# Performance work log

Hardware: AMD Instinct MI355X
Metric: run time of the kernel (lower is better)

The kernel has to match this reference:

```python
import jax, jax.numpy as jnp
import numpy as np
import math

L = 6; D = 768; NH = 12; DH = D // NH; V = 2048; CTX = 512; B = 16; T = 512
PAD_ID = 0; PAD_X = 18; PAD_Y = 32; N_ACTIONS = 9


def _layernorm(x, s, b, eps=1e-5):
    m = jnp.mean(x, axis=-1, keepdims=True)
    v = jnp.mean((x - m) ** 2, axis=-1, keepdims=True)
    return (x - m) * jax.lax.rsqrt(v + eps) * s + b


def setup_inputs() -> dict:
    key = jax.random.key(0)
    ks = jax.random.split(key, 16)
    s = 0.02
    x_emb = jax.random.normal(ks[4], (19, D), jnp.float32) * s
    x_emb = x_emb.at[PAD_X].set(0.0)  # padding_idx row is zero in torch
    y_emb = jax.random.normal(ks[5], (33, D), jnp.float32) * s
    y_emb = y_emb.at[PAD_Y].set(0.0)
    return {
        "history_cards": jax.random.randint(ks[0], (B, T), 0, V),
        "history_players": jax.random.randint(ks[1], (B, T), 0, 2),
        "deck": jax.random.randint(ks[2], (B, 8), 0, V),
        "opp_deck": jax.random.randint(ks[3], (B, 8), 0, V),
        "tok_emb": jax.random.normal(ks[6], (V, D), jnp.float32) * s,
        "player_emb": jax.random.normal(ks[7], (2, D), jnp.float32) * s,
        "pos_emb": jax.random.normal(ks[8], (CTX, D), jnp.float32) * s,
        "x_emb": x_emb,
        "y_emb": y_emb,
        "ln1_s": jnp.ones((L, D), jnp.float32),
        "ln1_b": jnp.zeros((L, D), jnp.float32),
        "qkv_w": jax.random.normal(ks[9], (L, D, 3 * D), jnp.float32) * s,
        "qkv_b": jnp.zeros((L, 3 * D), jnp.float32),
        "proj_w": jax.random.normal(ks[10], (L, D, D), jnp.float32) * s,
        "proj_b": jnp.zeros((L, D), jnp.float32),
        "ln2_s": jnp.ones((L, D), jnp.float32),
        "ln2_b": jnp.zeros((L, D), jnp.float32),
        "fc1_w": jax.random.normal(ks[11], (L, D, 4 * D), jnp.float32) * s,
        "fc1_b": jnp.zeros((L, 4 * D), jnp.float32),
        "fc2_w": jax.random.normal(ks[12], (L, 4 * D, D), jnp.float32) * s,
        "fc2_b": jnp.zeros((L, D), jnp.float32),
        "lnf_s": jnp.ones((D,), jnp.float32),
        "lnf_b": jnp.zeros((D,), jnp.float32),
        "head_w": jax.random.normal(ks[13], (D, N_ACTIONS), jnp.float32) * s,
        "head_b": jnp.zeros((N_ACTIONS,), jnp.float32),
    }


def reference(history_cards, history_players, deck, opp_deck,
              tok_emb, player_emb, pos_emb, x_emb, y_emb,
              ln1_s, ln1_b, qkv_w, qkv_b, proj_w, proj_b,
              ln2_s, ln2_b, fc1_w, fc1_b, fc2_w, fc2_b,
              lnf_s, lnf_b, head_w, head_b):
    Bc, Tc = history_cards.shape
    attn_mask = history_cards != PAD_ID                      # (B,T) True = valid
    all_pad = ~jnp.any(attn_mask, axis=1)
    attn_mask = attn_mask.at[:, 0].set(attn_mask[:, 0] | all_pad)

    # multi-embedding sum (history_x/history_y are None => padding rows = 0)
    h = (tok_emb[history_cards]
         + player_emb[jnp.clip(history_players, 0, 1)]
         + x_emb[PAD_X] + y_emb[PAD_Y]
         + jnp.mean(tok_emb[deck], axis=1, keepdims=True)
         + jnp.mean(tok_emb[opp_deck], axis=1, keepdims=True))
    x = h + pos_emb[:Tc][None]                               # (B,T,D)

    causal = jnp.tril(jnp.ones((Tc, Tc), bool))
    mask = causal[None, None, :, :] & attn_mask[:, None, None, :]  # (B,1,T,T)
    neg_inf = jnp.float32(-jnp.inf)
    scale = 1.0 / math.sqrt(DH)

    for i in range(L):
        # attention
        xn = _layernorm(x, ln1_s[i], ln1_b[i])
        qkv = xn @ qkv_w[i] + qkv_b[i]
        q, k, v = jnp.split(qkv, 3, axis=-1)
        q = q.reshape(Bc, Tc, NH, DH)
        k = k.reshape(Bc, Tc, NH, DH)
        v = v.reshape(Bc, Tc, NH, DH)
        scores = jnp.einsum('bihd,bjhd->bhij', q, k) * scale
        scores = jnp.where(mask, scores, neg_inf)
        w = jax.nn.softmax(scores, axis=-1)
        w = jnp.nan_to_num(w, nan=0.0, posinf=0.0, neginf=0.0)
        y = jnp.einsum('bhij,bjhd->bihd', w, v).reshape(Bc, Tc, D)
        x = x + (y @ proj_w[i] + proj_b[i])
        # MLP
        xn = _layernorm(x, ln2_s[i], ln2_b[i])
        hmid = jax.nn.gelu(xn @ fc1_w[i] + fc1_b[i], approximate=False)
        x = x + (hmid @ fc2_w[i] + fc2_b[i])

    x = _layernorm(x, lnf_s, lnf_b)
    last_idx = jnp.clip(jnp.sum(attn_mask.astype(jnp.int32), axis=1) - 1, 0, None)
    last_h = x[jnp.arange(Bc), last_idx]                     # (B,D)
    return last_h @ head_w + head_b                          # (B,9)
```

## Files before the change

### kernel.cpp

```cpp
#include <hip/hip_runtime.h>
#include <hip/hip_bf16.h>
#include <math.h>

typedef __hip_bfloat16 bf16;
typedef __bf16 bf16x8 __attribute__((ext_vector_type(8)));
typedef float f32x4 __attribute__((ext_vector_type(4)));

__device__ __forceinline__ float b2f(bf16 v){ return __bfloat162float(v); }
__device__ __forceinline__ bf16  f2b(float v){ return __float2bfloat16(v); }

__device__ __forceinline__ float gelu_f(float v){
    float y = v * (1.f + 0.044715f * v * v);
    return v / (1.f + __expf(-1.5957691216057308f * y));
}

__device__ __forceinline__ void gl_lds16(const bf16* g, bf16* l) {
    __builtin_amdgcn_global_load_lds((const __attribute__((address_space(1))) unsigned int*)g,
                                     (__attribute__((address_space(3))) unsigned int*)l, 16, 0, 0);
}

__device__ __forceinline__ uint2 pack4bf(const float* v){
    union { unsigned short e[4]; uint2 u; } pk;
    #pragma unroll
    for (int r = 0; r < 4; r++) pk.e[r] = __builtin_bit_cast(unsigned short, f2b(v[r]));
    return pk.u;
}

__device__ __forceinline__ void phase_bar() {
    __builtin_amdgcn_sched_barrier(0);
    __builtin_amdgcn_s_barrier();
    __builtin_amdgcn_sched_barrier(0);
}

__global__ __launch_bounds__(256) void deckmean_k(const int* __restrict__ deck, const int* __restrict__ opp,
                                                  const float* __restrict__ tok, float* __restrict__ deckm)
{
    int b = blockIdx.x, w = blockIdx.y;
    const int* dk = (w ? opp : deck) + b * 8;
    int idx[8];
    #pragma unroll
    for (int j = 0; j < 8; j++) idx[j] = dk[j];
    float* out = deckm + (size_t)(w * 16 + b) * 768;
    for (int d = threadIdx.x; d < 768; d += 256) {
        float s = 0.f;
        #pragma unroll
        for (int j = 0; j < 8; j++) s += tok[(size_t)idx[j] * 768 + d];
        out[d] = s * 0.125f;
    }
}

__global__ __launch_bounds__(512) void mask_k(const int* __restrict__ cards, int* __restrict__ maskb,
                                              int* __restrict__ lastidx)
{
    int b = blockIdx.x, t = threadIdx.x;
    int m = (cards[b * 512 + t] != 0) ? 1 : 0;
    maskb[b * 512 + t] = m;
    __shared__ int red[512];
    red[t] = m; __syncthreads();
    for (int st = 256; st > 0; st >>= 1) { if (t < st) red[t] += red[t + st]; __syncthreads(); }
    if (t == 0) {
        int cnt = red[0];
        if (cnt == 0) { maskb[b * 512] = 1; cnt = 1; }
        lastidx[b] = cnt - 1;
    }
}

__global__ __launch_bounds__(256) void embed_k(const int* __restrict__ cards, const int* __restrict__ players,
                                               const float* __restrict__ tok, const float* __restrict__ pemb,
                                               const float* __restrict__ pos, const float* __restrict__ deckm,
                                               float* __restrict__ x)
{
    int t = blockIdx.x;
    int b = t >> 9, ti = t & 511;
    int cd = cards[t];
    int p = players[t]; p = p < 0 ? 0 : (p > 1 ? 1 : p);
    const float* tr  = tok  + (size_t)cd * 768;
    const float* pr  = pemb + (size_t)p  * 768;
    const float* po  = pos  + (size_t)ti * 768;
    const float* dm = deckm + (size_t)b * 768;
    const float* om = deckm + (size_t)(16 + b) * 768;
    float* xr = x + (size_t)t * 768;
    for (int d = threadIdx.x; d < 768; d += 256)
        xr[d] = tr[d] + pr[d] + po[d] + dm[d] + om[d];
}

__global__ __launch_bounds__(192) void ln_k(const float* __restrict__ x, const float* __restrict__ s,
                                            const float* __restrict__ b, bf16* __restrict__ out)
{
    int row = blockIdx.x, tid = threadIdx.x;
    float4 v = ((const float4*)(x + (size_t)row * 768))[tid];
    float sum = v.x + v.y + v.z + v.w;
    float sq  = v.x * v.x + v.y * v.y + v.z * v.z + v.w * v.w;
    #pragma unroll
    for (int off = 32; off > 0; off >>= 1) {
        sum += __shfl_xor(sum, off, 64);
        sq  += __shfl_xor(sq,  off, 64);
    }
    __shared__ float red[6];
    int wv = tid >> 6;
    if ((tid & 63) == 0) { red[wv] = sum; red[3 + wv] = sq; }
    __syncthreads();
    float S = red[0] + red[1] + red[2];
    float Q = red[3] + red[4] + red[5];
    float mean = S * (1.f / 768.f);
    float var  = Q * (1.f / 768.f) - mean * mean;
    float rstd = rsqrtf(var + 1e-5f);
    float4 sv = ((const float4*)s)[tid];
    float4 bv = ((const float4*)b)[tid];
    float o[4] = { (v.x - mean) * rstd * sv.x + bv.x, (v.y - mean) * rstd * sv.y + bv.y,
                   (v.z - mean) * rstd * sv.z + bv.z, (v.w - mean) * rstd * sv.w + bv.w };
    ((uint2*)(out + (size_t)row * 768))[tid] = pack4bf(o);
}

__global__ __launch_bounds__(256) void transpose4_k(const float* __restrict__ qw, const float* __restrict__ pw,
                                                    const float* __restrict__ f1, const float* __restrict__ f2,
                                                    bf16* __restrict__ oq, bf16* __restrict__ op,
                                                    bf16* __restrict__ o1, bf16* __restrict__ o2)
{
    int t = blockIdx.x;
    const float* in; bf16* out; int K, N, nbx;
    if (t < 432)       { in = qw; out = oq; K = 768;  N = 2304; nbx = 36; }
    else if (t < 576)  { in = pw; out = op; K = 768;  N = 768;  t -= 432;  nbx = 12; }
    else if (t < 1152) { in = f1; out = o1; K = 768;  N = 3072; t -= 576;  nbx = 48; }
    else               { in = f2; out = o2; K = 3072; N = 768;  t -= 1152; nbx = 12; }
    int n0 = (t % nbx) * 64, k0 = (t / nbx) * 64;
    int kq = threadIdx.x & 15, nq = threadIdx.x >> 4;
    float4 rr[4];
    #pragma unroll
    for (int r = 0; r < 4; r++)
        rr[r] = *(const float4*)&in[(size_t)(k0 + kq * 4 + r) * N + n0 + nq * 4];
    const float* fp = (const float*)rr;
    #pragma unroll
    for (int c = 0; c < 4; c++) {
        float v[4] = { fp[c], fp[4 + c], fp[8 + c], fp[12 + c] };
        *(uint2*)&out[(size_t)(n0 + nq * 4 + c) * K + k0 + kq * 4] = pack4bf(v);
    }
}

__global__ __launch_bounds__(512, 2) void gemm256_k(const bf16* __restrict__ A, const bf16* __restrict__ BT,
                                                    const float* __restrict__ bias, bf16* __restrict__ out,
                                                    int N, int K, int act, int nbn)
{
    __shared__ __align__(16) bf16 As0[256 * 64];
    __shared__ __align__(16) bf16 As1[256 * 64];
    __shared__ __align__(16) bf16 Bs0[256 * 64];
    __shared__ __align__(16) bf16 Bs1[256 * 64];

    const int tid  = threadIdx.x;
    const int lane = tid & 63, wid = tid >> 6;
    const int quad = lane >> 4, l16 = lane & 15;
    const int wr = wid >> 2, wc = wid & 3;
    const int cg0 = quad ^ (l16 & 7);
    const int cg1 = cg0 ^ 4;

    const int nwg  = gridDim.x;
    const int wgid = ((int)blockIdx.x & 7) * (nwg >> 3) + ((int)blockIdx.x >> 3);
    const int mt = wgid / nbn, nt = wgid - mt * nbn;
    const int m0 = mt * 256, n0 = nt * 256;

    const int srow = wid * 8 + (lane >> 3);
    const int scg  = (lane & 7) ^ (lane >> 3);
    const bf16* sa[4]; const bf16* sb[4];
    #pragma unroll
    for (int s = 0; s < 4; s++) {
        sa[s] = A  + (size_t)(m0 + s * 64 + srow) * K + scg * 8;
        sb[s] = BT + (size_t)(n0 + s * 64 + srow) * K + scg * 8;
    }

#define STG_A2(s, DST) gl_lds16(sa[s], &DST[((s) * 64 + wid * 8) * 64])
#define STG_B2(s, DST) gl_lds16(sb[s], &DST[((s) * 64 + wid * 8) * 64])
#define ADV { _Pragma("unroll") for (int s = 0; s < 4; s++) { sa[s] += 64; sb[s] += 64; } }
#define LD_B2(BV, cg, BC) { _Pragma("unroll") for (int ni = 0; ni < 4; ni++) \
    BV[ni] = __builtin_bit_cast(bf16x8, *(const uint4*)&BC[(wc * 64 + ni * 16 + l16) * 64 + (cg) * 8]); }
#define LD_A2(rb, cg, AC) { _Pragma("unroll") for (int mi = 0; mi < 4; mi++) \
    afv[mi] = __builtin_bit_cast(bf16x8, *(const uint4*)&AC[(wr * 128 + (rb) + mi * 16 + l16) * 64 + (cg) * 8]); }
#define MFMA16(MB, BV) { _Pragma("unroll") for (int mi = 0; mi < 4; mi++) \
    _Pragma("unroll") for (int ni = 0; ni < 4; ni++) \
        acc[(MB) + mi][ni] = __builtin_amdgcn_mfma_f32_16x16x32_bf16(BV[ni], afv[mi], acc[(MB) + mi][ni], 0, 0, 0); }

#define TILE256(AC, BC, AN, BN, PF) { \
    LD_B2(bfv0, cg0, BC); LD_A2(0, cg0, AC); \
    if (PF) { STG_B2(0, BN); STG_B2(1, BN); STG_B2(2, BN); STG_B2(3, BN); } \
    phase_bar(); \
    __builtin_amdgcn_s_setprio(1); MFMA16(0, bfv0); __builtin_amdgcn_s_setprio(0); \
    phase_bar(); \
    LD_B2(bfv1, cg1, BC); LD_A2(0, cg1, AC); \
    if (PF) { STG_A2(0, AN); STG_A2(2, AN); } \
    phase_bar(); \
    __builtin_amdgcn_s_setprio(1); MFMA16(0, bfv1); __builtin_amdgcn_s_setprio(0); \
    phase_bar(); \
    LD_A2(64, cg0, AC); \
    if (PF) { STG_A2(1, AN); STG_A2(3, AN); ADV; } \
    phase_bar(); \
    __builtin_amdgcn_s_setprio(1); MFMA16(4, bfv0); __builtin_amdgcn_s_setprio(0); \
    phase_bar(); \
    LD_A2(64, cg1, AC); \
    phase_bar(); \
    __builtin_amdgcn_s_setprio(1); MFMA16(4, bfv1); __builtin_amdgcn_s_setprio(0); \
    if (PF) { asm volatile("s_waitcnt vmcnt(0)" ::: "memory"); } \
    phase_bar(); }

    f32x4 acc[8][4] = {};
    const int NKT = K >> 6;

    STG_B2(0, Bs0); STG_B2(1, Bs0); STG_B2(2, Bs0); STG_B2(3, Bs0);
    STG_A2(0, As0); STG_A2(1, As0); STG_A2(2, As0); STG_A2(3, As0);
    ADV;
    asm volatile("s_waitcnt vmcnt(0)" ::: "memory");
    phase_bar();

    bf16x8 bfv0[4], bfv1[4], afv[4];
    #pragma unroll 1
    for (int kt2 = 0; kt2 < NKT; kt2 += 2) {
        { const bool pf = true;
          TILE256(As0, Bs0, As1, Bs1, pf); }
        { const bool pf = (kt2 + 2 < NKT);
          TILE256(As1, Bs1, As0, Bs0, pf); }
    }

    float4 bv[4];
    #pragma unroll
    for (int ni = 0; ni < 4; ni++)
        bv[ni] = *(const float4*)&bias[n0 + wc * 64 + ni * 16 + quad * 4];

    #pragma unroll
    for (int mi = 0; mi < 8; mi++) {
        const int m = m0 + wr * 128 + mi * 16 + l16;
        #pragma unroll
        for (int ni = 0; ni < 4; ni++) {
            const int nb2 = n0 + wc * 64 + ni * 16 + quad * 4;
            float v[4] = { acc[mi][ni][0] + bv[ni].x, acc[mi][ni][1] + bv[ni].y,
                           acc[mi][ni][2] + bv[ni].z, acc[mi][ni][3] + bv[ni].w };
            if (act) {
                #pragma unroll
                for (int r = 0; r < 4; r++) v[r] = gelu_f(v[r]);
            }
            *(uint2*)&out[(size_t)m * N + nb2] = pack4bf(v);
        }
    }
#undef STG_A2
#undef STG_B2
#undef ADV
#undef LD_B2
#undef LD_A2
#undef MFMA16
#undef TILE256
}

__global__ __launch_bounds__(512, 2) void gemmn128_k(const bf16* __restrict__ A, const bf16* __restrict__ BT,
                                                     const float* __restrict__ bias, float* __restrict__ x,
                                                     int N, int K, int nbn)
{
    __shared__ __align__(16) bf16 NA0[256 * 64];
    __shared__ __align__(16) bf16 NA1[256 * 64];
    __shared__ __align__(16) bf16 NA2[256 * 64];
    __shared__ __align__(16) bf16 NB0[128 * 64];
    __shared__ __align__(16) bf16 NB1[128 * 64];
    __shared__ __align__(16) bf16 NB2[128 * 64];

    const int tid  = threadIdx.x;
    const int lane = tid & 63, wid = tid >> 6;
    const int quad = lane >> 4, l16 = lane & 15;
    const int wr = wid >> 1, wc = wid & 1;
    const int cg0 = quad ^ (l16 & 7);
    const int cg1 = cg0 ^ 4;

    const int nwg  = gridDim.x;
    const int wgid = ((int)blockIdx.x & 7) * (nwg >> 3) + ((int)blockIdx.x >> 3);
    const int mt = wgid / nbn, nt = wgid - mt * nbn;
    const int m0 = mt * 256, n0 = nt * 128;

    const int srow = wid * 8 + (lane >> 3);
    const int scg  = (lane & 7) ^ (lane >> 3);
    const bf16* sa[4]; const bf16* sb[2];
    #pragma unroll
    for (int s = 0; s < 4; s++) sa[s] = A  + (size_t)(m0 + s * 64 + srow) * K + scg * 8;
    #pragma unroll
    for (int s = 0; s < 2; s++) sb[s] = BT + (size_t)(n0 + s * 64 + srow) * K + scg * 8;

#define NSTG6(NA, NB) { \
    gl_lds16(sa[0], &NA[(0 * 64 + wid * 8) * 64]); gl_lds16(sa[1], &NA[(1 * 64 + wid * 8) * 64]); \
    gl_lds16(sa[2], &NA[(2 * 64 + wid * 8) * 64]); gl_lds16(sa[3], &NA[(3 * 64 + wid * 8) * 64]); \
    gl_lds16(sb[0], &NB[(0 * 64 + wid * 8) * 64]); gl_lds16(sb[1], &NB[(1 * 64 + wid * 8) * 64]); }
#define NADV { _Pragma("unroll") for (int s = 0; s < 4; s++) sa[s] += 64; sb[0] += 64; sb[1] += 64; }
#define NLD(cg, NA, NB) { _Pragma("unroll") for (int i = 0; i < 4; i++) { \
    bfv[i] = __builtin_bit_cast(bf16x8, *(const uint4*)&NB[(wc * 64 + i * 16 + l16) * 64 + (cg) * 8]); \
    afv[i] = __builtin_bit_cast(bf16x8, *(const uint4*)&NA[(wr * 64 + i * 16 + l16) * 64 + (cg) * 8]); } }
#define NMFMA { _Pragma("unroll") for (int mi = 0; mi < 4; mi++) \
    _Pragma("unroll") for (int ni = 0; ni < 4; ni++) \
        acc[mi][ni] = __builtin_amdgcn_mfma_f32_16x16x32_bf16(bfv[ni], afv[mi], acc[mi][ni], 0, 0, 0); }
#define NITER(NAc, NBc, NAs, NBs) { \
    const bool pf = (kt + 2 < NKT); \
    NLD(cg0, NAc, NBc); \
    if (pf) { NSTG6(NAs, NBs); NADV; } \
    phase_bar(); \
    __builtin_amdgcn_s_setprio(1); NMFMA; __builtin_amdgcn_s_setprio(0); \
    phase_bar(); \
    NLD(cg1, NAc, NBc); \
    phase_bar(); \
    __builtin_amdgcn_s_setprio(1); NMFMA; __builtin_amdgcn_s_setprio(0); \
    if (pf)               { asm volatile("s_waitcnt vmcnt(6)" ::: "memory"); phase_bar(); } \
    else if (kt + 1 < NKT){ asm volatile("s_waitcnt vmcnt(0)" ::: "memory"); phase_bar(); } \
    kt++; \
}

    f32x4 acc[4][4] = {};
    const int NKT = K >> 6;

    NSTG6(NA0, NB0); NADV;
    NSTG6(NA1, NB1); NADV;
    asm volatile("s_waitcnt vmcnt(6)" ::: "memory");
    phase_bar();

    int kt = 0;
    bf16x8 bfv[4], afv[4];
    #pragma unroll 1
    for (int kt3 = 0; kt3 < NKT; kt3 += 3) {
        NITER(NA0, NB0, NA2, NB2);
        NITER(NA1, NB1, NA0, NB0);
        NITER(NA2, NB2, NA1, NB1);
    }

    float4 bv4[4];
    #pragma unroll
    for (int ni = 0; ni < 4; ni++)
        bv4[ni] = *(const float4*)&bias[n0 + wc * 64 + ni * 16 + quad * 4];

    #pragma unroll
    for (int mi = 0; mi < 4; mi++) {
        const int m = m0 + wr * 64 + mi * 16 + l16;
        #pragma unroll
        for (int ni = 0; ni < 4; ni++) {
            const int nb2 = n0 + wc * 64 + ni * 16 + quad * 4;
            float* xp = &x[(size_t)m * N + nb2];
            float4 xo = *(float4*)xp;
            xo.x += acc[mi][ni][0] + bv4[ni].x;
            xo.y += acc[mi][ni][1] + bv4[ni].y;
            xo.z += acc[mi][ni][2] + bv4[ni].z;
            xo.w += acc[mi][ni][3] + bv4[ni].w;
            *(float4*)xp = xo;
        }
    }
#undef NSTG6
#undef NADV
#undef NLD
#undef NMFMA
#undef NITER
}

__global__ __launch_bounds__(256) void attn_k(const bf16* __restrict__ qkv, const int* __restrict__ mask,
                                              bf16* __restrict__ y)
{
    const int qt = blockIdx.x, h = blockIdx.y, b = blockIdx.z;
    const int qbase = qt * 128, tokb = b * 512;
    __shared__ __align__(16) unsigned short Kl[128][72];
    __shared__ __align__(16) unsigned short Vt[64][136];
    __shared__ __align__(16) unsigned short Ptq[4][16][136];
    __shared__ float mkf[128];

    const int tid = threadIdx.x, wave = tid >> 6, lane = tid & 63;
    const int quad = lane >> 4, l16 = lane & 15;

    bf16x8 bq[2][2];
    #pragma unroll
    for (int qc = 0; qc < 2; qc++) {
        const bf16* qp = &qkv[(size_t)(tokb + qbase + wave * 32 + qc * 16 + l16) * 2304 + h * 64];
        bq[qc][0] = __builtin_bit_cast(bf16x8, *(const uint4*)(qp + quad * 8));
        bq[qc][1] = __builtin_bit_cast(bf16x8, *(const uint4*)(qp + 32 + quad * 8));
    }

    float m_i[2] = { -INFINITY, -INFINITY }, l_i[2] = { 0.f, 0.f };
    f32x4 Oacc[2][4] = {};

    const int nst = qt + 1;
    for (int s = 0; s < nst; s++) {
        const int j0 = s * 128;
        __syncthreads();
        {
            int key = tid >> 1, c0 = (tid & 1) * 32;
            const bf16* kg = &qkv[(size_t)(tokb + j0 + key) * 2304 + 768  + h * 64 + c0];
            const bf16* vg = &qkv[(size_t)(tokb + j0 + key) * 2304 + 1536 + h * 64 + c0];
            #pragma unroll
            for (int q = 0; q < 4; q++)
                *(uint4*)&Kl[key][c0 + q * 8] = *(const uint4*)(kg + q * 8);
            union { uint4 u[4]; unsigned short e[32]; } vv;
            #pragma unroll
            for (int q = 0; q < 4; q++) vv.u[q] = *(const uint4*)(vg + q * 8);
            #pragma unroll
            for (int j = 0; j < 32; j++) Vt[c0 + j][key] = vv.e[j];
            if (tid < 128) mkf[tid] = mask[b * 512 + j0 + tid] ? 0.f : -INFINITY;
        }
        __syncthreads();

        #pragma unroll
        for (int qc = 0; qc < 2; qc++) {
            const int qi = qbase + wave * 32 + qc * 16 + l16;

            f32x4 sc[8] = {};
            #pragma unroll
            for (int kcc = 0; kcc < 8; kcc++) {
                bf16x8 af0 = __builtin_bit_cast(bf16x8, *(const uint4*)&Kl[kcc * 16 + l16][quad * 8]);
                bf16x8 af1 = __builtin_bit_cast(bf16x8, *(const uint4*)&Kl[kcc * 16 + l16][32 + quad * 8]);
                sc[kcc] = __builtin_amdgcn_mfma_f32_16x16x32_bf16(af0, bq[qc][0], sc[kcc], 0, 0, 0);
                sc[kcc] = __builtin_amdgcn_mfma_f32_16x16x32_bf16(af1, bq[qc][1], sc[kcc], 0, 0, 0);
            }

            float pv[8][4];
            float mx = -INFINITY;
            #pragma unroll
            for (int kcc = 0; kcc < 8; kcc++) {
                float4 mk4 = *(const float4*)&mkf[kcc * 16 + quad * 4];
                float mkr[4] = { mk4.x, mk4.y, mk4.z, mk4.w };
                #pragma unroll
                for (int r = 0; r < 4; r++) {
                    int krel = kcc * 16 + quad * 4 + r;
                    float sval = (j0 + krel <= qi) ? (sc[kcc][r] * 0.125f + mkr[r]) : -INFINITY;
                    pv[kcc][r] = sval;
                    mx = fmaxf(mx, sval);
                }
            }
            mx = fmaxf(mx, __shfl_xor(mx, 16, 64));
            mx = fmaxf(mx, __shfl_xor(mx, 32, 64));
            float mn = fmaxf(m_i[qc], mx);
            float alpha = (mn == -INFINITY) ? 1.f : __expf(m_i[qc] - mn);
            float lsum = 0.f;
            #pragma unroll
            for (int kcc = 0; kcc < 8; kcc++)
                #pragma unroll
                for (int r = 0; r < 4; r++) {
                    float pp = (pv[kcc][r] == -INFINITY) ? 0.f : __expf(pv[kcc][r] - mn);
                    pv[kcc][r] = pp; lsum += pp;
                }
            lsum += __shfl_xor(lsum, 16, 64);
            lsum += __shfl_xor(lsum, 32, 64);
            m_i[qc] = mn; l_i[qc] = alpha * l_i[qc] + lsum;

            #pragma unroll
            for (int kcc = 0; kcc < 8; kcc++)
                *(uint2*)&Ptq[wave][l16][kcc * 16 + quad * 4] = pack4bf(pv[kcc]);
            #pragma unroll
            for (int mc = 0; mc < 4; mc++)
                #pragma unroll
                for (int r = 0; r < 4; r++) Oacc[qc][mc][r] *= alpha;

            __syncthreads();

            #pragma unroll
            for (int kcc = 0; kcc < 4; kcc++) {
                bf16x8 pb = __builtin_bit_cast(bf16x8, *(const uint4*)&Ptq[wave][l16][kcc * 32 + quad * 8]);
                #pragma unroll
                for (int mc = 0; mc < 4; mc++) {
                    bf16x8 vf = __builtin_bit_cast(bf16x8, *(const uint4*)&Vt[mc * 16 + l16][kcc * 32 + quad * 8]);
                    Oacc[qc][mc] = __builtin_amdgcn_mfma_f32_16x16x32_bf16(vf, pb, Oacc[qc][mc], 0, 0, 0);
                }
            }
        }
    }

    #pragma unroll
    for (int qc = 0; qc < 2; qc++) {
        float inv = (l_i[qc] > 0.f) ? 1.f / l_i[qc] : 0.f;
        const int tok = tokb + qbase + wave * 32 + qc * 16 + l16;
        #pragma unroll
        for (int mc = 0; mc < 4; mc++) {
            float v[4] = { Oacc[qc][mc][0] * inv, Oacc[qc][mc][1] * inv,
                           Oacc[qc][mc][2] * inv, Oacc[qc][mc][3] * inv };
            *(uint2*)&y[(size_t)tok * 768 + h * 64 + mc * 16 + quad * 4] = pack4bf(v);
        }
    }
}

__global__ __launch_bounds__(256) void head_k(const float* __restrict__ x, const int* __restrict__ lastidx,
                                              const float* __restrict__ ls, const float* __restrict__ lb,
                                              const float* __restrict__ hw, const float* __restrict__ hb,
                                              float* __restrict__ out)
{
    int b = blockIdx.x, tid = threadIdx.x;
    const float* xr = x + ((size_t)(b * 512 + lastidx[b])) * 768;
    float v0 = xr[tid], v1 = xr[tid + 256], v2 = xr[tid + 512];
    __shared__ float rs[256], rq[256];
    rs[tid] = v0 + v1 + v2; rq[tid] = v0 * v0 + v1 * v1 + v2 * v2;
    __syncthreads();
    for (int st = 128; st > 0; st >>= 1) {
        if (tid < st) { rs[tid] += rs[tid + st]; rq[tid] += rq[tid + st]; }
        __syncthreads();
    }
    float mean = rs[0] * (1.f / 768.f);
    float var  = rq[0] * (1.f / 768.f) - mean * mean;
    float rstd = rsqrtf(var + 1e-5f);
    float part[9];
    #pragma unroll
    for (int a = 0; a < 9; a++) part[a] = 0.f;
    float vv[3] = { v0, v1, v2 };
    #pragma unroll
    for (int e = 0; e < 3; e++) {
        int d = tid + e * 256;
        float xnv = (vv[e] - mean) * rstd * ls[d] + lb[d];
        #pragma unroll
        for (int a = 0; a < 9; a++) part[a] += xnv * hw[d * 9 + a];
    }
    __shared__ float r9[9][256];
    #pragma unroll
    for (int a = 0; a < 9; a++) r9[a][tid] = part[a];
    __syncthreads();
    for (int st = 128; st > 0; st >>= 1) {
        if (tid < st) {
            for (int a = 0; a < 9; a++) r9[a][tid] += r9[a][tid + st];
        }
        __syncthreads();
    }
    if (tid < 9) out[b * 9 + tid] = r9[tid][0] + hb[tid];
}

extern "C" void kernel_launch(void* const* d_in, const int* in_sizes, int n_in,
                              void* d_out, int out_size, void* d_ws, size_t ws_size,
                              hipStream_t stream) {
    const int*   cards   = (const int*)  d_in[0];
    const int*   players = (const int*)  d_in[1];
    const int*   deck    = (const int*)  d_in[2];
    const int*   oppd    = (const int*)  d_in[3];
    const float* tok     = (const float*)d_in[4];
    const float* pemb    = (const float*)d_in[5];
    const float* pos     = (const float*)d_in[6];
    const float* ln1s  = (const float*)d_in[9];
    const float* ln1b  = (const float*)d_in[10];
    const float* qkvw  = (const float*)d_in[11];
    const float* qkvb  = (const float*)d_in[12];
    const float* projw = (const float*)d_in[13];
    const float* projb = (const float*)d_in[14];
    const float* ln2s  = (const float*)d_in[15];
    const float* ln2b  = (const float*)d_in[16];
    const float* fc1w  = (const float*)d_in[17];
    const float* fc1b  = (const float*)d_in[18];
    const float* fc2w  = (const float*)d_in[19];
    const float* fc2b  = (const float*)d_in[20];
    const float* lnfs  = (const float*)d_in[21];
    const float* lnfb  = (const float*)d_in[22];
    const float* hw    = (const float*)d_in[23];
    const float* hb    = (const float*)d_in[24];
    float* out = (float*)d_out;

    char* p = (char*)d_ws;
    auto alloc = [&](size_t bytes) { char* q = p; p += (bytes + 255) & ~((size_t)255); return q; };
    float* x     = (float*)alloc(8192ull * 768 * 4);
    bf16*  xn    = (bf16*) alloc(8192ull * 768 * 2);
    bf16*  big   = (bf16*) alloc(8192ull * 3072 * 2);
    bf16*  wt    = (bf16*) alloc(7077888ull * 2);
    float* deckm = (float*)alloc(2ull * 16 * 768 * 4);
    int*   maskb = (int*)  alloc(8192ull * 4);
    int*   lasti = (int*)  alloc(64);

    bf16* wq = wt;
    bf16* wp = wq + 2304ull * 768;
    bf16* w1 = wp + 768ull * 768;
    bf16* w2 = w1 + 3072ull * 768;

    deckmean_k<<<dim3(16, 2), 256, 0, stream>>>(deck, oppd, tok, deckm);
    mask_k<<<16, 512, 0, stream>>>(cards, maskb, lasti);
    embed_k<<<8192, 256, 0, stream>>>(cards, players, tok, pemb, pos, deckm, x);

    for (int i = 0; i < 6; i++) {
        transpose4_k<<<1728, 256, 0, stream>>>(
            qkvw + (size_t)i * 768 * 2304, projw + (size_t)i * 768 * 768,
            fc1w + (size_t)i * 768 * 3072, fc2w + (size_t)i * 3072 * 768,
            wq, wp, w1, w2);

        ln_k<<<8192, 192, 0, stream>>>(x, ln1s + i * 768, ln1b + i * 768, xn);
        gemm256_k<<<288, 512, 0, stream>>>(xn, wq, qkvb + i * 2304, big, 2304, 768, 0, 9);
        attn_k<<<dim3(4, 12, 16), 256, 0, stream>>>(big, maskb, xn);
        gemmn128_k<<<192, 512, 0, stream>>>(xn, wp, projb + i * 768, x, 768, 768, 6);
        ln_k<<<8192, 192, 0, stream>>>(x, ln2s + i * 768, ln2b + i * 768, xn);
        gemm256_k<<<384, 512, 0, stream>>>(xn, w1, fc1b + i * 3072, big, 3072, 768, 1, 12);
        gemmn128_k<<<192, 512, 0, stream>>>(big, w2, fc2b + i * 768, x, 768, 3072, 6);
    }

    head_k<<<16, 256, 0, stream>>>(x, lasti, lnfs, lnfb, hw, hb, out);
}
```

Before: 1.920 ms.

## Replace 256x256 QKV/FC1 GEMM with 256x128 triple-buffered bf16-output kernel

The QKV and FC1 GEMMs move from a 256x256 double-buffered tile kernel to a 256x128 tile kernel with three LDS stages and partial vmcnt waits, so loads for the next tile overlap compute. This doubles the workgroup count (576 and 768 instead of 288 and 384), which gives better occupancy and wave balance across the compute units with M=8192. The cost is lower per-tile arithmetic intensity and more global traffic for A.

```diff
diff --git a/kernel.cpp b/kernel.cpp
--- a/kernel.cpp
+++ b/kernel.cpp
@@ -137,100 +137,93 @@
     }
 }
 
-__global__ __launch_bounds__(512, 2) void gemm256_k(const bf16* __restrict__ A, const bf16* __restrict__ BT,
-                                                    const float* __restrict__ bias, bf16* __restrict__ out,
-                                                    int N, int K, int act, int nbn)
-{
-    __shared__ __align__(16) bf16 As0[256 * 64];
-    __shared__ __align__(16) bf16 As1[256 * 64];
-    __shared__ __align__(16) bf16 Bs0[256 * 64];
-    __shared__ __align__(16) bf16 Bs1[256 * 64];
+__global__ __launch_bounds__(512, 2) void gemmn128b_k(const bf16* __restrict__ A, const bf16* __restrict__ BT,
+                                                      const float* __restrict__ bias, bf16* __restrict__ out,
+                                                      int N, int K, int act, int nbn)
+{
+    __shared__ __align__(16) bf16 MA0[256 * 64];
+    __shared__ __align__(16) bf16 MA1[256 * 64];
+    __shared__ __align__(16) bf16 MA2[256 * 64];
+    __shared__ __align__(16) bf16 MB0[128 * 64];
+    __shared__ __align__(16) bf16 MB1[128 * 64];
+    __shared__ __align__(16) bf16 MB2[128 * 64];
 
     const int tid  = threadIdx.x;
     const int lane = tid & 63, wid = tid >> 6;
     const int quad = lane >> 4, l16 = lane & 15;
-    const int wr = wid >> 2, wc = wid & 3;
+    const int wr = wid >> 1, wc = wid & 1;
     const int cg0 = quad ^ (l16 & 7);
     const int cg1 = cg0 ^ 4;
 
     const int nwg  = gridDim.x;
     const int wgid = ((int)blockIdx.x & 7) * (nwg >> 3) + ((int)blockIdx.x >> 3);
     const int mt = wgid / nbn, nt = wgid - mt * nbn;
-    const int m0 = mt * 256, n0 = nt * 256;
+    const int m0 = mt * 256, n0 = nt * 128;
 
     const int srow = wid * 8 + (lane >> 3);
     const int scg  = (lane & 7) ^ (lane >> 3);
-    const bf16* sa[4]; const bf16* sb[4];
-    #pragma unroll
-    for (int s = 0; s < 4; s++) {
-        sa[s] = A  + (size_t)(m0 + s * 64 + srow) * K + scg * 8;
-        sb[s] = BT + (size_t)(n0 + s * 64 + srow) * K + scg * 8;
-    }
-
-#define STG_A2(s, DST) gl_lds16(sa[s], &DST[((s) * 64 + wid * 8) * 64])
-#define STG_B2(s, DST) gl_lds16(sb[s], &DST[((s) * 64 + wid * 8) * 64])
-#define ADV { _Pragma("unroll") for (int s = 0; s < 4; s++) { sa[s] += 64; sb[s] += 64; } }
-#define LD_B2(BV, cg, BC) { _Pragma("unroll") for (int ni = 0; ni < 4; ni++) \
-    BV[ni] = __builtin_bit_cast(bf16x8, *(const uint4*)&BC[(wc * 64 + ni * 16 + l16) * 64 + (cg) * 8]); }
-#define LD_A2(rb, cg, AC) { _Pragma("unroll") for (int mi = 0; mi < 4; mi++) \
-    afv[mi] = __builtin_bit_cast(bf16x8, *(const uint4*)&AC[(wr * 128 + (rb) + mi * 16 + l16) * 64 + (cg) * 8]); }
-#define MFMA16(MB, BV) { _Pragma("unroll") for (int mi = 0; mi < 4; mi++) \
+    const bf16* sa[4]; const bf16* sb[2];
+    #pragma unroll
+    for (int s = 0; s < 4; s++) sa[s] = A  + (size_t)(m0 + s * 64 + srow) * K + scg * 8;
+    #pragma unroll
+    for (int s = 0; s < 2; s++) sb[s] = BT + (size_t)(n0 + s * 64 + srow) * K + scg * 8;
+
+#define MSTG6(NA, NB) { \
+    gl_lds16(sa[0], &NA[(0 * 64 + wid * 8) * 64]); gl_lds16(sa[1], &NA[(1 * 64 + wid * 8) * 64]); \
+    gl_lds16(sa[2], &NA[(2 * 64 + wid * 8) * 64]); gl_lds16(sa[3], &NA[(3 * 64 + wid * 8) * 64]); \
+    gl_lds16(sb[0], &NB[(0 * 64 + wid * 8) * 64]); gl_lds16(sb[1], &NB[(1 * 64 + wid * 8) * 64]); }
+#define MADV { _Pragma("unroll") for (int s = 0; s < 4; s++) sa[s] += 64; sb[0] += 64; sb[1] += 64; }
+#define MLD(cg, NA, NB) { _Pragma("unroll") for (int i = 0; i < 4; i++) { \
+    bfv[i] = __builtin_bit_cast(bf16x8, *(const uint4*)&NB[(wc * 64 + i * 16 + l16) * 64 + (cg) * 8]); \
+    afv[i] = __builtin_bit_cast(bf16x8, *(const uint4*)&NA[(wr * 64 + i * 16 + l16) * 64 + (cg) * 8]); } }
+#define MMFMA { _Pragma("unroll") for (int mi = 0; mi < 4; mi++) \
     _Pragma("unroll") for (int ni = 0; ni < 4; ni++) \
-        acc[(MB) + mi][ni] = __builtin_amdgcn_mfma_f32_16x16x32_bf16(BV[ni], afv[mi], acc[(MB) + mi][ni], 0, 0, 0); }
-
-#define TILE256(AC, BC, AN, BN, PF) { \
-    LD_B2(bfv0, cg0, BC); LD_A2(0, cg0, AC); \
-    if (PF) { STG_B2(0, BN); STG_B2(1, BN); STG_B2(2, BN); STG_B2(3, BN); } \
+        acc[mi][ni] = __builtin_amdgcn_mfma_f32_16x16x32_bf16(bfv[ni], afv[mi], acc[mi][ni], 0, 0, 0); }
+#define MITER(NAc, NBc, NAs, NBs) { \
+    const bool pf = (kt + 2 < NKT); \
+    MLD(cg0, NAc, NBc); \
+    if (pf) { MSTG6(NAs, NBs); MADV; } \
     phase_bar(); \
-    __builtin_amdgcn_s_setprio(1); MFMA16(0, bfv0); __builtin_amdgcn_s_setprio(0); \
+    __builtin_amdgcn_s_setprio(1); MMFMA; __builtin_amdgcn_s_setprio(0); \
     phase_bar(); \
-    LD_B2(bfv1, cg1, BC); LD_A2(0, cg1, AC); \
-    if (PF) { STG_A2(0, AN); STG_A2(2, AN); } \
+    MLD(cg1, NAc, NBc); \
     phase_bar(); \
-    __builtin_amdgcn_s_setprio(1); MFMA16(0, bfv1); __builtin_amdgcn_s_setprio(0); \
-    phase_bar(); \
-    LD_A2(64, cg0, AC); \
-    if (PF) { STG_A2(1, AN); STG_A2(3, AN); ADV; } \
-    phase_bar(); \
-    __builtin_amdgcn_s_setprio(1); MFMA16(4, bfv0); __builtin_amdgcn_s_setprio(0); \
-    phase_bar(); \
-    LD_A2(64, cg1, AC); \
-    phase_bar(); \
-    __builtin_amdgcn_s_setprio(1); MFMA16(4, bfv1); __builtin_amdgcn_s_setprio(0); \
-    if (PF) { asm volatile("s_waitcnt vmcnt(0)" ::: "memory"); } \
-    phase_bar(); }
-
-    f32x4 acc[8][4] = {};
+    __builtin_amdgcn_s_setprio(1); MMFMA; __builtin_amdgcn_s_setprio(0); \
+    if (pf)               { asm volatile("s_waitcnt vmcnt(6)" ::: "memory"); phase_bar(); } \
+    else if (kt + 1 < NKT){ asm volatile("s_waitcnt vmcnt(0)" ::: "memory"); phase_bar(); } \
+    kt++; \
+}
+
+    f32x4 acc[4][4] = {};
     const int NKT = K >> 6;
 
-    STG_B2(0, Bs0); STG_B2(1, Bs0); STG_B2(2, Bs0); STG_B2(3, Bs0);
-    STG_A2(0, As0); STG_A2(1, As0); STG_A2(2, As0); STG_A2(3, As0);
-    ADV;
-    asm volatile("s_waitcnt vmcnt(0)" ::: "memory");
+    MSTG6(MA0, MB0); MADV;
+    MSTG6(MA1, MB1); MADV;
+    asm volatile("s_waitcnt vmcnt(6)" ::: "memory");
     phase_bar();
 
-    bf16x8 bfv0[4], bfv1[4], afv[4];
+    int kt = 0;
+    bf16x8 bfv[4], afv[4];
     #pragma unroll 1
-    for (int kt2 = 0; kt2 < NKT; kt2 += 2) {
-        { const bool pf = true;
-          TILE256(As0, Bs0, As1, Bs1, pf); }
-        { const bool pf = (kt2 + 2 < NKT);
-          TILE256(As1, Bs1, As0, Bs0, pf); }
-    }
-
-    float4 bv[4];
+    for (int kt3 = 0; kt3 < NKT; kt3 += 3) {
+        MITER(MA0, MB0, MA2, MB2);
+        MITER(MA1, MB1, MA0, MB0);
+        MITER(MA2, MB2, MA1, MB1);
+    }
+
+    float4 bv4[4];
     #pragma unroll
     for (int ni = 0; ni < 4; ni++)
-        bv[ni] = *(const float4*)&bias[n0 + wc * 64 + ni * 16 + quad * 4];
-
-    #pragma unroll
-    for (int mi = 0; mi < 8; mi++) {
-        const int m = m0 + wr * 128 + mi * 16 + l16;
+        bv4[ni] = *(const float4*)&bias[n0 + wc * 64 + ni * 16 + quad * 4];
+
+    #pragma unroll
+    for (int mi = 0; mi < 4; mi++) {
+        const int m = m0 + wr * 64 + mi * 16 + l16;
         #pragma unroll
         for (int ni = 0; ni < 4; ni++) {
             const int nb2 = n0 + wc * 64 + ni * 16 + quad * 4;
-            float v[4] = { acc[mi][ni][0] + bv[ni].x, acc[mi][ni][1] + bv[ni].y,
-                           acc[mi][ni][2] + bv[ni].z, acc[mi][ni][3] + bv[ni].w };
+            float v[4] = { acc[mi][ni][0] + bv4[ni].x, acc[mi][ni][1] + bv4[ni].y,
+                           acc[mi][ni][2] + bv4[ni].z, acc[mi][ni][3] + bv4[ni].w };
             if (act) {
                 #pragma unroll
                 for (int r = 0; r < 4; r++) v[r] = gelu_f(v[r]);
@@ -238,13 +231,11 @@
             *(uint2*)&out[(size_t)m * N + nb2] = pack4bf(v);
         }
     }
-#undef STG_A2
-#undef STG_B2
-#undef ADV
-#undef LD_B2
-#undef LD_A2
-#undef MFMA16
-#undef TILE256
+#undef MSTG6
+#undef MADV
+#undef MLD
+#undef MMFMA
+#undef MITER
 }
 
 __global__ __launch_bounds__(512, 2) void gemmn128_k(const bf16* __restrict__ A, const bf16* __restrict__ BT,
@@ -566,11 +557,11 @@
             wq, wp, w1, w2);
 
         ln_k<<<8192, 192, 0, stream>>>(x, ln1s + i * 768, ln1b + i * 768, xn);
-        gemm256_k<<<288, 512, 0, stream>>>(xn, wq, qkvb + i * 2304, big, 2304, 768, 0, 9);
+        gemmn128b_k<<<576, 512, 0, stream>>>(xn, wq, qkvb + i * 2304, big, 2304, 768, 0, 18);
         attn_k<<<dim3(4, 12, 16), 256, 0, stream>>>(big, maskb, xn);
         gemmn128_k<<<192, 512, 0, stream>>>(xn, wp, projb + i * 768, x, 768, 768, 6);
         ln_k<<<8192, 192, 0, stream>>>(x, ln2s + i * 768, ln2b + i * 768, xn);
-        gemm256_k<<<384, 512, 0, stream>>>(xn, w1, fc1b + i * 3072, big, 3072, 768, 1, 12);
+        gemmn128b_k<<<768, 512, 0, stream>>>(xn, w1, fc1b + i * 3072, big, 3072, 768, 1, 24);
         gemmn128_k<<<192, 512, 0, stream>>>(big, w2, fc2b + i * 768, x, 768, 3072, 6);
     }
 
```

New measurement: 1.910 ms. Within noise of the previous version (-0.5%).
